# Optimization experiments

Hardware: AMD Instinct MI355X
Metric: run time of the kernel (lower is better)

The kernel has to match this reference:

```python
import jax, jax.numpy as jnp
import numpy as np

DIM = 64
NUM_HEAD = 8
SIZES = [3, 5, 7]
GROUPS = [2, 1, 1]
G_DIM = DIM // 4
SPLITS = [G_DIM * n for n in GROUPS]  # [32, 16, 16]


def _dwconv(x, w, k):
    # depthwise conv, NCHW, kernel (C,1,k,k), groups=C, same padding
    return jax.lax.conv_general_dilated(
        x, w, window_strides=(1, 1), padding=[(k // 2, k // 2)] * 2,
        dimension_numbers=('NCHW', 'OIHW', 'NCHW'),
        feature_group_count=x.shape[1])


def _conv1x1(x, w):
    # w: (out, in)
    return jnp.einsum('oi,bihw->bohw', w, x)


def _avgpool2(x):
    b, c, h, w = x.shape
    return x.reshape(b, c, h // 2, 2, w // 2, 2).mean(axis=(3, 5))


def _l2norm(x, eps=1e-12):
    n = jnp.sqrt(jnp.sum(x * x, axis=-1, keepdims=True))
    return x / jnp.maximum(n, eps)


def setup_inputs() -> dict:
    key = jax.random.key(0)
    ks = jax.random.split(key, 20)
    s = 0.05
    inp = {
        'x': jax.random.normal(ks[0], (4, DIM, 256, 256), dtype=jnp.float32),
        'y': jax.random.normal(ks[1], (4, DIM, 256, 256), dtype=jnp.float32),
    }
    i = 2
    for pfx in ('hp1', 'hp2'):
        for kk, ch in zip(SIZES, SPLITS):
            inp[f'{pfx}_w{kk}'] = jax.random.normal(ks[i], (ch, 1, kk, kk), dtype=jnp.float32) * s
            i += 1
    for name in ('qh_w', 'kh_w', 'vh_w', 'ql_w', 'kl_w', 'vl_w', 'proj_w'):
        inp[name] = jax.random.normal(ks[i], (DIM, DIM), dtype=jnp.float32) * s
        i += 1
    inp['attn_w1'] = jax.random.normal(ks[i], (DIM // 4, DIM), dtype=jnp.float32) * s; i += 1
    inp['attn_w2'] = jax.random.normal(ks[i], (DIM, DIM // 4), dtype=jnp.float32) * s; i += 1
    inp['temperature'] = jnp.ones((NUM_HEAD, 1, 1), dtype=jnp.float32)
    return inp


def reference(x, y, hp1_w3, hp1_w5, hp1_w7, hp2_w3, hp2_w5, hp2_w7,
              qh_w, kh_w, vh_w, ql_w, kl_w, vl_w, proj_w,
              attn_w1, attn_w2, temperature):
    b, c, h, w = x.shape
    idx = np.cumsum(SPLITS)[:-1].tolist()
    xs = jnp.split(x, idx, axis=1)
    ys = jnp.split(y, idx, axis=1)
    hp1 = [hp1_w3, hp1_w5, hp1_w7]
    hp2 = [hp2_w3, hp2_w5, hp2_w7]
    x_h = jnp.concatenate([_dwconv(xs[i], hp1[i], SIZES[i]) for i in range(3)], axis=1)
    y_h = jnp.concatenate([_dwconv(ys[i], hp2[i], SIZES[i]) for i in range(3)], axis=1)
    q_h = _conv1x1(x_h, qh_w)
    k_h = _conv1x1(y_h, kh_w)
    v_h = _conv1x1(x_h, vh_w)
    pooled = jnp.mean(q_h * k_h, axis=(2, 3), keepdims=True)  # b,c,1,1
    high_att = jnp.tanh(_conv1x1(jax.nn.relu(_conv1x1(pooled, attn_w1)), attn_w2))
    out_h = high_att * v_h
    q_l = _conv1x1(_avgpool2(x), ql_w)
    k_l = _conv1x1(_avgpool2(y), kl_w)
    v_l = _conv1x1(y, vl_w)
    ch = c // NUM_HEAD
    q_l = q_l.reshape(b, NUM_HEAD, ch, -1)  # b head c (h/2*w/2)
    k_l = k_l.reshape(b, NUM_HEAD, ch, -1)
    v_l = v_l.reshape(b, NUM_HEAD, ch, -1)  # b head c (h*w)
    q_l = _l2norm(q_l)
    k_l = _l2norm(k_l)
    low_att = jnp.einsum('bhcn,bhdn->bhcd', q_l, k_l) * temperature
    low_att = jax.nn.softmax(low_att, axis=-1)
    out_l = jnp.einsum('bhcd,bhdn->bhcn', low_att, v_l).reshape(b, c, h, w)
    return _conv1x1(out_h + out_l, proj_w)
```

## Files before the change

### kernel.cpp

```cpp
#include <hip/hip_runtime.h>
#include <hip/hip_bf16.h>
#include <math.h>

#define NPX   65536
#define IMGST 4194304
#define NB    4

template<int K, int RT>
__device__ __forceinline__ void dw_strip(const float* __restrict__ in,
                                         const float* __restrict__ wp,
                                         float* __restrict__ outp,
                                         int rowS, int c4) {
    float w[K * K];
#pragma unroll
    for (int i = 0; i < K * K; ++i) w[i] = wp[i];

    float acc[RT][4];
#pragma unroll
    for (int i = 0; i < RT; ++i)
#pragma unroll
        for (int j = 0; j < 4; ++j) acc[i][j] = 0.f;

    const bool lok = (c4 != 0);
    const bool rok = (c4 < 252);
    const int off0 = lok ? -4 : 0;
    const int off2 = rok ? 4 : 0;

#pragma unroll
    for (int ri = 0; ri < RT + K - 1; ++ri) {
        const int gr = rowS - K / 2 + ri;
        float v[12];
        if ((unsigned)gr < 256u) {
            const float* rp = in + gr * 256 + c4;
            const float4 m0 = *reinterpret_cast<const float4*>(rp + off0);
            const float4 m1 = *reinterpret_cast<const float4*>(rp);
            const float4 m2 = *reinterpret_cast<const float4*>(rp + off2);
            v[0] = lok ? m0.x : 0.f; v[1] = lok ? m0.y : 0.f;
            v[2] = lok ? m0.z : 0.f; v[3] = lok ? m0.w : 0.f;
            v[4] = m1.x; v[5] = m1.y; v[6] = m1.z; v[7] = m1.w;
            v[8] = rok ? m2.x : 0.f;  v[9] = rok ? m2.y : 0.f;
            v[10] = rok ? m2.z : 0.f; v[11] = rok ? m2.w : 0.f;
        } else {
#pragma unroll
            for (int t = 0; t < 12; ++t) v[t] = 0.f;
        }
#pragma unroll
        for (int i = 0; i < RT; ++i) {
            const int dy = ri - i;
            if (dy >= 0 && dy < K) {
#pragma unroll
                for (int dx = 0; dx < K; ++dx) {
                    const float wv = w[dy * K + dx];
#pragma unroll
                    for (int j = 0; j < 4; ++j)
                        acc[i][j] = fmaf(wv, v[j + dx + 4 - K / 2], acc[i][j]);
                }
            }
        }
    }

    float* obase = outp + (size_t)rowS * 256 + c4;
#pragma unroll
    for (int i = 0; i < RT; ++i) {
        float4 o;
        o.x = acc[i][0]; o.y = acc[i][1]; o.z = acc[i][2]; o.w = acc[i][3];
        *reinterpret_cast<float4*>(obase + i * 256) = o;
    }
}

__global__ __launch_bounds__(256) void dsattn_dwconv2(
        const float* __restrict__ xin, const float* __restrict__ yin,
        float* __restrict__ xout, float* __restrict__ yout,
        const float* __restrict__ x3, const float* __restrict__ x5,
        const float* __restrict__ x7, const float* __restrict__ y3,
        const float* __restrict__ y5, const float* __restrict__ y7) {
    const int tid = threadIdx.x;
    const int xb = blockIdx.x;
    const int sel = blockIdx.y >> 2;
    const int b   = blockIdx.y & 3;
    const int tc = tid & 63, tr = tid >> 6;
    const int c4 = tc * 4;

    const float* inb = (sel == 0 ? xin : yin) + (size_t)b * IMGST;
    float* outb      = (sel == 0 ? xout : yout) + (size_t)b * IMGST;

    if (xb < 512) {
        const int c = xb >> 4, band = xb & 15;
        const float* w = (sel == 0 ? x3 : y3) + c * 9;
        dw_strip<3, 4>(inb + (size_t)c * NPX, w, outb + (size_t)c * NPX,
                       band * 16 + tr * 4, c4);
    } else if (xb < 768) {
        const int u = xb - 512;
        const int c = 32 + (u >> 4), band = u & 15;
        const float* w = (sel == 0 ? x5 : y5) + (c - 32) * 25;
        dw_strip<5, 4>(inb + (size_t)c * NPX, w, outb + (size_t)c * NPX,
                       band * 16 + tr * 4, c4);
    } else {
        const int u = xb - 768;
        const int c = 48 + (u >> 5), band = u & 31;
        const float* w = (sel == 0 ? x7 : y7) + (c - 48) * 49;
        dw_strip<7, 2>(inb + (size_t)c * NPX, w, outb + (size_t)c * NPX,
                       band * 8 + tr * 2, c4);
    }
}

__global__ __launch_bounds__(256) void dsattn_crossgram(
        const float* __restrict__ xh, const float* __restrict__ yh,
        float* __restrict__ Spart) {
    __shared__ float sx[64 * 65];
    __shared__ float sy[64 * 65];
    const int tid = threadIdx.x;
    const int chunk = blockIdx.x;
    const int b = blockIdx.y;
    const int rt = tid >> 4;
    const int ct = tid & 15;
    float acc[16];
#pragma unroll
    for (int i = 0; i < 16; ++i) acc[i] = 0.f;
    const size_t ibase = (size_t)b * IMGST + chunk * 512;

    for (int tile = 0; tile < 8; ++tile) {
        __syncthreads();
        for (int idx = tid; idx < 4096; idx += 256) {
            const int c = idx >> 6, p = idx & 63;
            const size_t g = ibase + (size_t)c * NPX + tile * 64 + p;
            sx[p * 65 + c] = xh[g];
            sy[p * 65 + c] = yh[g];
        }
        __syncthreads();
        for (int p = 0; p < 64; ++p) {
            float xr[4], yc[4];
#pragma unroll
            for (int j = 0; j < 4; ++j) {
                xr[j] = sx[p * 65 + rt * 4 + j];
                yc[j] = sy[p * 65 + ct * 4 + j];
            }
#pragma unroll
            for (int r = 0; r < 4; ++r)
#pragma unroll
                for (int c2 = 0; c2 < 4; ++c2)
                    acc[r * 4 + c2] = fmaf(xr[r], yc[c2], acc[r * 4 + c2]);
        }
    }
    float* outp = Spart + ((size_t)b * 128 + chunk) * 4096;
#pragma unroll
    for (int r = 0; r < 4; ++r)
#pragma unroll
        for (int c2 = 0; c2 < 4; ++c2)
            outp[(rt * 4 + r) * 64 + ct * 4 + c2] = acc[r * 4 + c2];
}

__global__ __launch_bounds__(256) void dsattn_reduceS(
        const float* __restrict__ Spart, float* __restrict__ Sred) {
    const int i = blockIdx.x * 256 + threadIdx.x;
    const int b = blockIdx.y;
    const float* p = Spart + (size_t)b * 128 * 4096 + i;
    float s = 0.f;
#pragma unroll 4
    for (int k = 0; k < 128; ++k) s += p[(size_t)k * 4096];
    Sred[b * 4096 + i] = s;
}

__global__ __launch_bounds__(256) void dsattn_poolgram(
        const float* __restrict__ x, const float* __restrict__ y,
        float* __restrict__ Ppart) {
    __shared__ float sx[64 * 65];
    __shared__ float sy[64 * 65];
    const int tid = threadIdx.x;
    const int irow = blockIdx.x;
    const int b = blockIdx.y;
    const int rt = tid >> 4, ct = tid & 15;
    float aXY[16], aXX[16], aYY[16];
#pragma unroll
    for (int i = 0; i < 16; ++i) { aXY[i] = 0.f; aXX[i] = 0.f; aYY[i] = 0.f; }
    const size_t ibase = (size_t)b * IMGST + (size_t)(2 * irow) * 256;

    for (int tile = 0; tile < 2; ++tile) {
        __syncthreads();
        for (int idx = tid; idx < 4096; idx += 256) {
            const int c = idx >> 6, jj = idx & 63;
            const size_t g = ibase + (size_t)c * NPX + 2 * (tile * 64 + jj);
            const float* px0 = x + g;
            const float* py0 = y + g;
            sx[jj * 65 + c] = 0.25f * (px0[0] + px0[1] + px0[256] + px0[257]);
            sy[jj * 65 + c] = 0.25f * (py0[0] + py0[1] + py0[256] + py0[257]);
        }
        __syncthreads();
        for (int p = 0; p < 64; ++p) {
            float xr[4], xc[4], yr[4], yc[4];
#pragma unroll
            for (int j = 0; j < 4; ++j) {
                xr[j] = sx[p * 65 + rt * 4 + j];
                xc[j] = sx[p * 65 + ct * 4 + j];
                yr[j] = sy[p * 65 + rt * 4 + j];
                yc[j] = sy[p * 65 + ct * 4 + j];
            }
#pragma unroll
            for (int r = 0; r < 4; ++r)
#pragma unroll
                for (int c2 = 0; c2 < 4; ++c2) {
                    aXY[r * 4 + c2] = fmaf(xr[r], yc[c2], aXY[r * 4 + c2]);
                    aXX[r * 4 + c2] = fmaf(xr[r], xc[c2], aXX[r * 4 + c2]);
                    aYY[r * 4 + c2] = fmaf(yr[r], yc[c2], aYY[r * 4 + c2]);
                }
        }
    }
    float* outp = Ppart + ((size_t)b * 128 + irow) * 12288;
#pragma unroll
    for (int r = 0; r < 4; ++r)
#pragma unroll
        for (int c2 = 0; c2 < 4; ++c2) {
            const int o = (rt * 4 + r) * 64 + ct * 4 + c2;
            outp[o]        = aXY[r * 4 + c2];
            outp[4096 + o] = aXX[r * 4 + c2];
            outp[8192 + o] = aYY[r * 4 + c2];
        }
}

__global__ __launch_bounds__(256) void dsattn_reduceP(
        const float* __restrict__ Ppart, float* __restrict__ Pred) {
    const int i = blockIdx.x * 256 + threadIdx.x;
    const int b = blockIdx.y;
    const float* p = Ppart + (size_t)b * 128 * 12288 + i;
    float s = 0.f;
#pragma unroll 4
    for (int k = 0; k < 128; ++k) s += p[(size_t)k * 12288];
    Pred[b * 12288 + i] = s;
}

__global__ __launch_bounds__(256) void dsattn_sandwich(
        const float* __restrict__ Pred, const float* __restrict__ Sred,
        const float* __restrict__ wql, const float* __restrict__ wkl,
        const float* __restrict__ wq,  const float* __restrict__ wk,
        float* __restrict__ nq2g, float* __restrict__ nk2g,
        float* __restrict__ Gg, float* __restrict__ pooledg) {
    __shared__ float Wl[64 * 65];
    __shared__ float Sl[64 * 65];
    __shared__ float Tl[64 * 65];
    __shared__ float red[256];
    const int unit = blockIdx.x, b = blockIdx.y, tid = threadIdx.x;
    const float *W1, *W2, *Sg;
    if (unit == 0)      { W1 = wql; W2 = wql; Sg = Pred + (size_t)b * 12288 + 4096; }
    else if (unit == 1) { W1 = wkl; W2 = wkl; Sg = Pred + (size_t)b * 12288 + 8192; }
    else if (unit == 2) { W1 = wql; W2 = wkl; Sg = Pred + (size_t)b * 12288; }
    else                { W1 = wq;  W2 = wk;  Sg = Sred + (size_t)b * 4096; }

    for (int i = tid; i < 4096; i += 256) {
        const int r = i >> 6, c = i & 63;
        Wl[r * 65 + c] = W1[i];
        Sl[r * 65 + c] = Sg[i];
    }
    __syncthreads();

    const int rt = tid >> 4, ct = tid & 15;
    float acc[16];
#pragma unroll
    for (int i = 0; i < 16; ++i) acc[i] = 0.f;
    for (int cc = 0; cc < 64; ++cc) {
        float wr[4], sc[4];
#pragma unroll
        for (int j = 0; j < 4; ++j) {
            wr[j] = Wl[(rt * 4 + j) * 65 + cc];
            sc[j] = Sl[cc * 65 + ct * 4 + j];
        }
#pragma unroll
        for (int r = 0; r < 4; ++r)
#pragma unroll
            for (int c2 = 0; c2 < 4; ++c2)
                acc[r * 4 + c2] = fmaf(wr[r], sc[c2], acc[r * 4 + c2]);
    }
#pragma unroll
    for (int r = 0; r < 4; ++r)
#pragma unroll
        for (int c2 = 0; c2 < 4; ++c2)
            Tl[(rt * 4 + r) * 65 + ct * 4 + c2] = acc[r * 4 + c2];
    __syncthreads();
    for (int i = tid; i < 4096; i += 256) Sl[(i >> 6) * 65 + (i & 63)] = W2[i];
    __syncthreads();

    if (unit == 2) {
        for (int i = tid; i < 512; i += 256) {
            const int h = i >> 6, r = (i >> 3) & 7, d = i & 7;
            float s = 0.f;
#pragma unroll
            for (int c = 0; c < 64; ++c)
                s = fmaf(Tl[(h * 8 + r) * 65 + c], Sl[(h * 8 + d) * 65 + c], s);
            Gg[b * 512 + i] = s;
        }
    } else {
        const int r = tid >> 2, part = tid & 3;
        float s = 0.f;
#pragma unroll
        for (int q = 0; q < 16; ++q) {
            const int cp = part * 16 + q;
            s = fmaf(Tl[r * 65 + cp], Sl[r * 65 + cp], s);
        }
        red[tid] = s;
        __syncthreads();
        if (tid < 64) {
            const float v = red[tid * 4] + red[tid * 4 + 1] + red[tid * 4 + 2] + red[tid * 4 + 3];
            if (unit == 0)      nq2g[b * 64 + tid] = v;
            else if (unit == 1) nk2g[b * 64 + tid] = v;
            else                pooledg[b * 64 + tid] = v * (1.f / 65536.f);
        }
    }
}

__global__ __launch_bounds__(256) void dsattn_smallmid(
        const float* __restrict__ nq2g, const float* __restrict__ nk2g,
        const float* __restrict__ Gg, const float* __restrict__ pooledg,
        const float* __restrict__ temp, const float* __restrict__ w1,
        const float* __restrict__ w2, const float* __restrict__ wvl,
        float* __restrict__ hattg, float* __restrict__ tvlg) {
    __shared__ float att[512];
    __shared__ float z[16];
    const int b = blockIdx.x, tid = threadIdx.x;
    if (tid < 16) {
        float a = 0.f;
#pragma unroll
        for (int c = 0; c < 64; ++c) a = fmaf(w1[tid * 64 + c], pooledg[b * 64 + c], a);
        z[tid] = fmaxf(a, 0.f);
    }
    if (tid < 64) {
        const int h = tid >> 3;
        const float tpr = temp[h];
        const float nq = fmaxf(sqrtf(nq2g[b * 64 + tid]), 1e-12f);
        float a[8], m = -1e30f;
#pragma unroll
        for (int d = 0; d < 8; ++d) {
            const float nk = fmaxf(sqrtf(nk2g[b * 64 + h * 8 + d]), 1e-12f);
            a[d] = Gg[b * 512 + tid * 8 + d] / (nq * nk) * tpr;
            m = fmaxf(m, a[d]);
        }
        float ssum = 0.f;
#pragma unroll
        for (int d = 0; d < 8; ++d) { a[d] = expf(a[d] - m); ssum += a[d]; }
        const float inv = 1.f / ssum;
#pragma unroll
        for (int d = 0; d < 8; ++d) att[tid * 8 + d] = a[d] * inv;
    }
    __syncthreads();
    if (tid < 64) {
        float a = 0.f;
#pragma unroll
        for (int i = 0; i < 16; ++i) a = fmaf(w2[tid * 16 + i], z[i], a);
        hattg[b * 64 + tid] = tanhf(a);
    }
    for (int i = tid; i < 4096; i += 256) {
        const int m = i >> 6, c = i & 63, h = m >> 3;
        float s = 0.f;
#pragma unroll
        for (int d = 0; d < 8; ++d) s = fmaf(att[m * 8 + d], wvl[(h * 8 + d) * 64 + c], s);
        tvlg[b * 4096 + i] = s;
    }
}

__global__ __launch_bounds__(256) void dsattn_fold(
        const float* __restrict__ wproj, const float* __restrict__ wvh,
        const float* __restrict__ hattg, const float* __restrict__ tvlg,
        float* __restrict__ At, float* __restrict__ Bt) {
    __shared__ float Pl[64 * 65];
    __shared__ float Vl[64 * 65];
    __shared__ float hm[64];
    const int unit = blockIdx.x, b = blockIdx.y, tid = threadIdx.x;
    if (tid < 64) hm[tid] = hattg[b * 64 + tid];
    for (int i = tid; i < 4096; i += 256) Pl[(i >> 6) * 65 + (i & 63)] = wproj[i];
    __syncthreads();
    for (int i = tid; i < 4096; i += 256) {
        const int m = i >> 6, c = i & 63;
        Vl[m * 65 + c] = (unit == 0) ? hm[m] * wvh[i] : tvlg[b * 4096 + i];
    }
    __syncthreads();

    const int rt = tid >> 4, ct = tid & 15;
    float acc[16];
#pragma unroll
    for (int i = 0; i < 16; ++i) acc[i] = 0.f;
    for (int m = 0; m < 64; ++m) {
        float pv[4], vv[4];
#pragma unroll
        for (int j = 0; j < 4; ++j) {
            pv[j] = Pl[(ct * 4 + j) * 65 + m];
            vv[j] = Vl[m * 65 + rt * 4 + j];
        }
#pragma unroll
        for (int r = 0; r < 4; ++r)
#pragma unroll
            for (int c2 = 0; c2 < 4; ++c2)
                acc[r * 4 + c2] = fmaf(pv[c2], vv[r], acc[r * 4 + c2]);
    }
    float* outp = ((unit == 0) ? At : Bt) + (size_t)b * 4096;
#pragma unroll
    for (int r = 0; r < 4; ++r)
#pragma unroll
        for (int c2 = 0; c2 < 4; ++c2)
            outp[(rt * 4 + r) * 64 + ct * 4 + c2] = acc[r * 4 + c2];
}

__global__ __launch_bounds__(256, 4) void dsattn_final(
        const float* __restrict__ xh, const float* __restrict__ y,
        const float* __restrict__ At, const float* __restrict__ Bt,
        float* __restrict__ out) {
    const int tid = threadIdx.x;
    const int b = blockIdx.y;
    const int lane = tid & 63;
    const int oc0 = __builtin_amdgcn_readfirstlane((tid >> 6) * 16);
    const size_t base = (size_t)b * IMGST + (size_t)blockIdx.x * 256 + lane * 4;
    const float* __restrict__ Ab = At + b * 4096 + oc0;
    const float* __restrict__ Bb = Bt + b * 4096 + oc0;

    float acc[16][4];
#pragma unroll
    for (int j = 0; j < 16; ++j)
#pragma unroll
        for (int k = 0; k < 4; ++k) acc[j][k] = 0.f;

#pragma unroll 2
    for (int c = 0; c < 64; ++c) {
        const float4 xv = *reinterpret_cast<const float4*>(xh + base + (size_t)c * NPX);
        const float4 yv = *reinterpret_cast<const float4*>(y  + base + (size_t)c * NPX);
#pragma unroll
        for (int j = 0; j < 16; ++j) {
            const float a  = Ab[c * 64 + j];
            const float bb = Bb[c * 64 + j];
            acc[j][0] = fmaf(a, xv.x, acc[j][0]);
            acc[j][1] = fmaf(a, xv.y, acc[j][1]);
            acc[j][2] = fmaf(a, xv.z, acc[j][2]);
            acc[j][3] = fmaf(a, xv.w, acc[j][3]);
            acc[j][0] = fmaf(bb, yv.x, acc[j][0]);
            acc[j][1] = fmaf(bb, yv.y, acc[j][1]);
            acc[j][2] = fmaf(bb, yv.z, acc[j][2]);
            acc[j][3] = fmaf(bb, yv.w, acc[j][3]);
        }
    }

    float* op = out + base;
#pragma unroll
    for (int j = 0; j < 16; ++j) {
        float4 v;
        v.x = acc[j][0]; v.y = acc[j][1]; v.z = acc[j][2]; v.w = acc[j][3];
        *reinterpret_cast<float4*>(op + (size_t)(oc0 + j) * NPX) = v;
    }
}

extern "C" void kernel_launch(void* const* d_in, const int* in_sizes, int n_in,
                              void* d_out, int out_size, void* d_ws, size_t ws_size,
                              hipStream_t stream) {
    const float* x      = (const float*)d_in[0];
    const float* y      = (const float*)d_in[1];
    const float* hp1_w3 = (const float*)d_in[2];
    const float* hp1_w5 = (const float*)d_in[3];
    const float* hp1_w7 = (const float*)d_in[4];
    const float* hp2_w3 = (const float*)d_in[5];
    const float* hp2_w5 = (const float*)d_in[6];
    const float* hp2_w7 = (const float*)d_in[7];
    const float* qh_w   = (const float*)d_in[8];
    const float* kh_w   = (const float*)d_in[9];
    const float* vh_w   = (const float*)d_in[10];
    const float* ql_w   = (const float*)d_in[11];
    const float* kl_w   = (const float*)d_in[12];
    const float* vl_w   = (const float*)d_in[13];
    const float* proj_w = (const float*)d_in[14];
    const float* attn_w1 = (const float*)d_in[15];
    const float* attn_w2 = (const float*)d_in[16];
    const float* temperature = (const float*)d_in[17];

    float* out = (float*)d_out;

    float* xh     = (float*)d_ws;
    float* Spart  = xh + (size_t)NB * IMGST;
    float* small  = Spart + (size_t)4 * 128 * 4096;
    float* Sred   = small;
    float* Pred   = Sred + 16384;
    float* nq2    = Pred + 49152;
    float* nk2    = nq2 + 256;
    float* G      = nk2 + 256;
    float* pooled = G + 2048;
    float* hatt   = pooled + 256;
    float* tvl    = hatt + 256;
    float* At     = tvl + 16384;
    float* Bt     = At + 16384;

    float* yh    = out;
    float* Ppart = out;

    dsattn_dwconv2<<<dim3(1280, 8), 256, 0, stream>>>(x, y, xh, yh,
                                                      hp1_w3, hp1_w5, hp1_w7,
                                                      hp2_w3, hp2_w5, hp2_w7);
    dsattn_crossgram<<<dim3(128, 4), 256, 0, stream>>>(xh, yh, Spart);
    dsattn_reduceS<<<dim3(16, 4), 256, 0, stream>>>(Spart, Sred);
    dsattn_poolgram<<<dim3(128, 4), 256, 0, stream>>>(x, y, Ppart);
    dsattn_reduceP<<<dim3(48, 4), 256, 0, stream>>>(Ppart, Pred);
    dsattn_sandwich<<<dim3(4, 4), 256, 0, stream>>>(Pred, Sred, ql_w, kl_w, qh_w, kh_w,
                                                    nq2, nk2, G, pooled);
    dsattn_smallmid<<<4, 256, 0, stream>>>(nq2, nk2, G, pooled, temperature,
                                           attn_w1, attn_w2, vl_w, hatt, tvl);
    dsattn_fold<<<dim3(2, 4), 256, 0, stream>>>(proj_w, vh_w, hatt, tvl, At, Bt);
    dsattn_final<<<dim3(256, 4), 256, 0, stream>>>(xh, y, At, Bt, out);
}
```

Measured before the change: 267.6 us.

## Remap dwconv blocks per XCD and vectorize gram-kernel global loads

Reorders the depthwise-conv block index so that the heavy 7x7 work is scheduled first and spread evenly across the eight XCDs (blockIdx & 7), which is meant to balance load and improve L2 locality. It also switches the cross-gram tile loads to float4 and the avg-pool loads to float2, cutting the number of global load instructions. The XCD mapping relies on round-robin dispatch and assumes the grid width is a multiple of eight.

```diff
diff --git a/kernel.cpp b/kernel.cpp
--- a/kernel.cpp
+++ b/kernel.cpp
@@ -75,7 +75,8 @@
         const float* __restrict__ x7, const float* __restrict__ y3,
         const float* __restrict__ y5, const float* __restrict__ y7) {
     const int tid = threadIdx.x;
-    const int xb = blockIdx.x;
+    const int xcd = blockIdx.x & 7;
+    const int v   = blockIdx.x >> 3;
     const int sel = blockIdx.y >> 2;
     const int b   = blockIdx.y & 3;
     const int tc = tid & 63, tr = tid >> 6;
@@ -84,23 +85,24 @@
     const float* inb = (sel == 0 ? xin : yin) + (size_t)b * IMGST;
     float* outb      = (sel == 0 ? xout : yout) + (size_t)b * IMGST;
 
-    if (xb < 512) {
-        const int c = xb >> 4, band = xb & 15;
+    if (v < 64) {
+        const int idx = xcd * 64 + v;
+        const int c = 48 + (idx >> 5), band = idx & 31;
+        const float* w = (sel == 0 ? x7 : y7) + (c - 48) * 49;
+        dw_strip<7, 2>(inb + (size_t)c * NPX, w, outb + (size_t)c * NPX,
+                       band * 8 + tr * 2, c4);
+    } else if (v < 128) {
+        const int idx = xcd * 64 + (v - 64);
+        const int c = idx >> 4, band = idx & 15;
         const float* w = (sel == 0 ? x3 : y3) + c * 9;
         dw_strip<3, 4>(inb + (size_t)c * NPX, w, outb + (size_t)c * NPX,
                        band * 16 + tr * 4, c4);
-    } else if (xb < 768) {
-        const int u = xb - 512;
-        const int c = 32 + (u >> 4), band = u & 15;
+    } else {
+        const int idx = xcd * 32 + (v - 128);
+        const int c = 32 + (idx >> 4), band = idx & 15;
         const float* w = (sel == 0 ? x5 : y5) + (c - 32) * 25;
         dw_strip<5, 4>(inb + (size_t)c * NPX, w, outb + (size_t)c * NPX,
                        band * 16 + tr * 4, c4);
-    } else {
-        const int u = xb - 768;
-        const int c = 48 + (u >> 5), band = u & 31;
-        const float* w = (sel == 0 ? x7 : y7) + (c - 48) * 49;
-        dw_strip<7, 2>(inb + (size_t)c * NPX, w, outb + (size_t)c * NPX,
-                       band * 8 + tr * 2, c4);
     }
 }
 
@@ -121,11 +123,15 @@
 
     for (int tile = 0; tile < 8; ++tile) {
         __syncthreads();
-        for (int idx = tid; idx < 4096; idx += 256) {
-            const int c = idx >> 6, p = idx & 63;
-            const size_t g = ibase + (size_t)c * NPX + tile * 64 + p;
-            sx[p * 65 + c] = xh[g];
-            sy[p * 65 + c] = yh[g];
+        for (int idx = tid; idx < 1024; idx += 256) {
+            const int c = idx >> 4, p4 = (idx & 15) * 4;
+            const size_t g = ibase + (size_t)c * NPX + tile * 64 + p4;
+            const float4 vx = *reinterpret_cast<const float4*>(&xh[g]);
+            const float4 vy = *reinterpret_cast<const float4*>(&yh[g]);
+            sx[(p4 + 0) * 65 + c] = vx.x; sx[(p4 + 1) * 65 + c] = vx.y;
+            sx[(p4 + 2) * 65 + c] = vx.z; sx[(p4 + 3) * 65 + c] = vx.w;
+            sy[(p4 + 0) * 65 + c] = vy.x; sy[(p4 + 1) * 65 + c] = vy.y;
+            sy[(p4 + 2) * 65 + c] = vy.z; sy[(p4 + 3) * 65 + c] = vy.w;
         }
         __syncthreads();
         for (int p = 0; p < 64; ++p) {
@@ -180,10 +186,12 @@
         for (int idx = tid; idx < 4096; idx += 256) {
             const int c = idx >> 6, jj = idx & 63;
             const size_t g = ibase + (size_t)c * NPX + 2 * (tile * 64 + jj);
-            const float* px0 = x + g;
-            const float* py0 = y + g;
-            sx[jj * 65 + c] = 0.25f * (px0[0] + px0[1] + px0[256] + px0[257]);
-            sy[jj * 65 + c] = 0.25f * (py0[0] + py0[1] + py0[256] + py0[257]);
+            const float2 a0 = *reinterpret_cast<const float2*>(x + g);
+            const float2 a1 = *reinterpret_cast<const float2*>(x + g + 256);
+            const float2 b0 = *reinterpret_cast<const float2*>(y + g);
+            const float2 b1 = *reinterpret_cast<const float2*>(y + g + 256);
+            sx[jj * 65 + c] = 0.25f * (a0.x + a0.y + a1.x + a1.y);
+            sy[jj * 65 + c] = 0.25f * (b0.x + b0.y + b1.x + b1.y);
         }
         __syncthreads();
         for (int p = 0; p < 64; ++p) {
```

Measured after the change: 259.8 us. -2.9%, faster.
